# Kernel optimization log

Hardware: AMD Instinct MI355X
Metric: run time of the kernel (lower is better)

The kernel has to match this reference:

```python
import jax, jax.numpy as jnp
import numpy as np

IN_DIM, HID_DIM, OUT_DIM, HEADS = 128, 256, 128, 4
N0, N1, N2 = 80000, 40000, 8000
E1, E2 = 400000, 128000
NEG_SLOPE = 0.2


def _glorot(key, shape):
    fan = shape[0] + shape[-1]
    lim = jnp.sqrt(6.0 / fan)
    return jax.random.uniform(key, shape, jnp.float32, -lim, lim)


def setup_inputs() -> dict:
    key = jax.random.key(0)
    ks = jax.random.split(key, 16)
    inp = {
        "x": jax.random.normal(ks[0], (N0, IN_DIM), jnp.float32),
        "edge_src1": jax.random.randint(ks[1], (E1,), 0, N0),
        "edge_dst1": jax.random.randint(ks[2], (E1,), 0, N1),
        "edge_src2": jax.random.randint(ks[3], (E2,), 0, N1),
        "edge_dst2": jax.random.randint(ks[4], (E2,), 0, N2),
        # GAT1: in_dim -> heads*in_dim (shared lin for src/dst in PyG when in_channels is int)
        "W1": _glorot(ks[5], (IN_DIM, HEADS * IN_DIM)),
        "att_src1": _glorot(ks[6], (HEADS, IN_DIM)),
        "att_dst1": _glorot(ks[7], (HEADS, IN_DIM)),
        "b1": jnp.zeros((HEADS * IN_DIM,), jnp.float32),
        # GAT2: hid_dim -> hid_dim, heads=1
        "W2": _glorot(ks[8], (HID_DIM, HID_DIM)),
        "att_src2": _glorot(ks[9], (1, HID_DIM)),
        "att_dst2": _glorot(ks[10], (1, HID_DIM)),
        "b2": jnp.zeros((HID_DIM,), jnp.float32),
        # Conv1d kernel_size=1 == per-node linear
        "conv1_w": _glorot(ks[11], (HID_DIM, HEADS * IN_DIM)),
        "conv1_b": jnp.zeros((HID_DIM,), jnp.float32),
        "conv2_w": _glorot(ks[12], (OUT_DIM, HID_DIM)),
        "conv2_b": jnp.zeros((OUT_DIM,), jnp.float32),
    }
    return inp


def _gat(x_src, x_dst, src, dst, W, att_s, att_d, bias, n_dst, heads, out_c):
    h_src = (x_src @ W).reshape(-1, heads, out_c)   # [Ns,H,C]
    h_dst = (x_dst @ W).reshape(-1, heads, out_c)   # [Nd,H,C]
    a_s = jnp.einsum('nhc,hc->nh', h_src, att_s)    # [Ns,H]
    a_d = jnp.einsum('nhc,hc->nh', h_dst, att_d)    # [Nd,H]
    alpha = jax.nn.leaky_relu(a_s[src] + a_d[dst], NEG_SLOPE)  # [E,H]
    m = jax.ops.segment_max(alpha, dst, num_segments=n_dst)
    alpha = jnp.exp(alpha - jnp.maximum(m, -1e30)[dst])
    denom = jax.ops.segment_sum(alpha, dst, num_segments=n_dst)
    alpha = alpha / (denom[dst] + 1e-16)
    msg = h_src[src] * alpha[:, :, None]            # [E,H,C]
    out = jax.ops.segment_sum(msg, dst, num_segments=n_dst)
    return out.reshape(n_dst, heads * out_c) + bias


def reference(x, edge_src1, edge_dst1, edge_src2, edge_dst2,
              W1, att_src1, att_dst1, b1, W2, att_src2, att_dst2, b2,
              conv1_w, conv1_b, conv2_w, conv2_b):
    # layer 0: GAT1 (heads=4, concat) + Conv1d(512->256, k=1)
    h = _gat(x, x[:N1], edge_src1, edge_dst1, W1, att_src1, att_dst1, b1,
             N1, HEADS, IN_DIM)                      # [N1, 512]
    h = h @ conv1_w.T + conv1_b                      # [N1, 256]
    # layer 1: GAT2 (heads=1) + Conv1d(256->128, k=1)
    h = _gat(h, h[:N2], edge_src2, edge_dst2, W2, att_src2, att_dst2, b2,
             N2, 1, HID_DIM)                         # [N2, 256]
    h = h @ conv2_w.T + conv2_b                      # [N2, 128]
    return h
```

## Files before the change

kernel.cpp:

```cpp
#include <hip/hip_runtime.h>
#include <math.h>

#define IN_DIM 128
#define HID_DIM 256
#define OUT_DIM 128
#define HEADS 4
#define N0 80000
#define N1 40000
#define N2 8000
#define E1 400000
#define E2 128000
#define NEG 0.2f
#define NB1 40
#define NB2 8
#define ZERO_BLKS 47
#define PH0_BLKS (ZERO_BLKS + 4)
#define PREP_BLKS 644
#define CAST_BLKS 1250
#define HIST_BLKS 2063
#define PH1_BLKS (PREP_BLKS + CAST_BLKS + HIST_BLKS)

typedef __attribute__((ext_vector_type(8))) short bf16x8;
typedef __attribute__((ext_vector_type(4))) float f32x4;

__device__ __forceinline__ float bf2f(short s) {
  return __uint_as_float(((unsigned int)(unsigned short)s) << 16);
}
__device__ __forceinline__ short f2bf(float f) {
  unsigned int u = __float_as_uint(f);
  unsigned int r = (u + 0x7FFFu + ((u >> 16) & 1u)) >> 16;
  return (short)r;
}
__device__ __forceinline__ float lrelu(float t) {
  return t > 0.f ? t : NEG * t;
}

__global__ __launch_bounds__(256) void phase0_kernel(
    float4* __restrict__ zp, const float* __restrict__ W1,
    const float* __restrict__ att_s1, const float* __restrict__ att_d1,
    float* __restrict__ p1) {
  int b = blockIdx.x, t = threadIdx.x;
  if (b < ZERO_BLKS) {
    int i = b * 256 + t;
    if (i < 12000) zp[i] = make_float4(0.f, 0.f, 0.f, 0.f);
  } else {
    int g = (b - ZERO_BLKS) * 256 + t;
    int i = g >> 3, hh = g & 7;
    int h = hh & 3;
    const float* att = (hh < 4) ? att_s1 : att_d1;
    float acc = 0.f;
    for (int c = 0; c < 128; c++)
      acc += W1[(long)i * 512 + h * 128 + c] * att[h * 128 + c];
    p1[g] = acc;
  }
}

__global__ __launch_bounds__(256) void phase1_kernel(
    const float* __restrict__ W1, const float* __restrict__ b1,
    const float* __restrict__ c1w, const float* __restrict__ c1b,
    const float* __restrict__ W2, const float* __restrict__ att_s2,
    const float* __restrict__ att_d2, const float* __restrict__ b2,
    const float* __restrict__ c2w, const float* __restrict__ c2b,
    short* __restrict__ M1t, const float* __restrict__ p1,
    float* __restrict__ bias1p, short* __restrict__ M2t,
    float* __restrict__ p2, float* __restrict__ bias2p,
    const float* __restrict__ x, short* __restrict__ x_bf,
    float* __restrict__ a_s, float* __restrict__ a_d,
    const int* __restrict__ ed1, const int* __restrict__ ed2,
    int* __restrict__ deg1, int* __restrict__ deg2, int* __restrict__ rank1,
    int* __restrict__ rank2) {
  int b = blockIdx.x, t = threadIdx.x;
  if (b < PREP_BLKS) {
    if (b < 512) {
      int g = b * 256 + t;
      int o = g >> 9, kf = g & 511;
      int h = kf >> 7, k = kf & 127;
      float acc = 0.f;
      for (int c = 0; c < 128; c++)
        acc +=
            W1[(long)k * 512 + h * 128 + c] * c1w[(long)o * 512 + h * 128 + c];
      M1t[g] = f2bf(acc);
    } else if (b < 640) {
      int g = (b - 512) * 256 + t;
      int o = g >> 8, k = g & 255;
      float acc = 0.f;
      for (int c = 0; c < 256; c++)
        acc += W2[(long)k * 256 + c] * c2w[(long)o * 256 + c];
      M2t[g] = f2bf(acc);
    } else if (b == 640) {
      if (t < 256) {
        float acc = c1b[t];
        for (int c = 0; c < 512; c++) acc += b1[c] * c1w[(long)t * 512 + c];
        bias1p[t] = acc;
      }
    } else if (b < 643) {
      int g = (b - 641) * 256 + t;
      if (g < 512) {
        int k = g >> 1, j = g & 1;
        const float* att = j ? att_d2 : att_s2;
        float acc = 0.f;
        for (int c = 0; c < 256; c++) acc += W2[(long)k * 256 + c] * att[c];
        p2[g] = acc;
      }
    } else {
      if (t < 128) {
        float acc = c2b[t];
        for (int c = 0; c < 256; c++) acc += b2[c] * c2w[(long)t * 256 + c];
        bias2p[t] = acc;
      }
    }
  } else if (b < PREP_BLKS + CAST_BLKS) {
    int bb = b - PREP_BLKS;
    int l16 = t & 15;
    long nb = ((long)bb * 16 + (t >> 4)) * 4;
    int ch0 = l16 * 8;
    float xs[4][8];
#pragma unroll
    for (int i = 0; i < 4; i++) {
      float4 a = *(const float4*)&x[(nb + i) * 128 + ch0];
      float4 bv = *(const float4*)&x[(nb + i) * 128 + ch0 + 4];
      xs[i][0] = a.x; xs[i][1] = a.y; xs[i][2] = a.z; xs[i][3] = a.w;
      xs[i][4] = bv.x; xs[i][5] = bv.y; xs[i][6] = bv.z; xs[i][7] = bv.w;
    }
#pragma unroll
    for (int i = 0; i < 4; i++) {
      short4 o1, o2;
      o1.x = f2bf(xs[i][0]); o1.y = f2bf(xs[i][1]);
      o1.z = f2bf(xs[i][2]); o1.w = f2bf(xs[i][3]);
      o2.x = f2bf(xs[i][4]); o2.y = f2bf(xs[i][5]);
      o2.z = f2bf(xs[i][6]); o2.w = f2bf(xs[i][7]);
      *(short4*)&x_bf[(nb + i) * 128 + ch0] = o1;
      *(short4*)&x_bf[(nb + i) * 128 + ch0 + 4] = o2;
    }
    float acc[4][8] = {};
#pragma unroll
    for (int c = 0; c < 8; c++) {
      float4 pA = *(const float4*)&p1[(ch0 + c) * 8];
      float4 pB = *(const float4*)&p1[(ch0 + c) * 8 + 4];
#pragma unroll
      for (int i = 0; i < 4; i++) {
        float xc = xs[i][c];
        acc[i][0] += xc * pA.x; acc[i][1] += xc * pA.y;
        acc[i][2] += xc * pA.z; acc[i][3] += xc * pA.w;
        acc[i][4] += xc * pB.x; acc[i][5] += xc * pB.y;
        acc[i][6] += xc * pB.z; acc[i][7] += xc * pB.w;
      }
    }
#pragma unroll
    for (int off = 1; off <= 8; off <<= 1) {
#pragma unroll
      for (int i = 0; i < 4; i++)
#pragma unroll
        for (int k = 0; k < 8; k++) acc[i][k] += __shfl_xor(acc[i][k], off);
    }
    if (l16 == 0) {
#pragma unroll
      for (int i = 0; i < 4; i++) {
        long n = nb + i;
        *(float4*)&a_s[n * 4] =
            make_float4(acc[i][0], acc[i][1], acc[i][2], acc[i][3]);
        if (n < N1)
          *(float4*)&a_d[n * 4] =
              make_float4(acc[i][4], acc[i][5], acc[i][6], acc[i][7]);
      }
    }
  } else {
    int e = (b - PREP_BLKS - CAST_BLKS) * 256 + t;
    if (e < E1) {
      rank1[e] = atomicAdd(&deg1[ed1[e]], 1);
    } else {
      int e2 = e - E1;
      if (e2 < E2) rank2[e2] = atomicAdd(&deg2[ed2[e2]], 1);
    }
  }
}

template<bool BIAS, bool OUTBF>
__global__ __launch_bounds__(256) void mm_bf16_kernel(
    const short* __restrict__ A, const short* __restrict__ Bt,
    const float* __restrict__ bias, void* __restrict__ Cv,
    int M, int N, int K) {
  __shared__ short As[128][72];
  __shared__ short Bs[64][72];
  int tid = threadIdx.x;
  int bn = blockIdx.x * 64;
  int bm = blockIdx.y * 128;
  int w = tid >> 6;
  int lane = tid & 63;
  int lr = lane & 15, kb = lane >> 4;
  f32x4 acc[2][4] = {};

  for (int k0 = 0; k0 < K; k0 += 64) {
#pragma unroll
    for (int i = 0; i < 4; i++) {
      int seg = tid + i * 256;
      int row = seg >> 3, part = seg & 7;
      int gm = bm + row;
      bf16x8 v = {0, 0, 0, 0, 0, 0, 0, 0};
      if (gm < M) v = *(const bf16x8*)(A + (long)gm * K + k0 + part * 8);
      *(bf16x8*)&As[row][part * 8] = v;
    }
#pragma unroll
    for (int i = 0; i < 2; i++) {
      int seg = tid + i * 256;
      int r = seg >> 3, part = seg & 7;
      *(bf16x8*)&Bs[r][part * 8] =
          *(const bf16x8*)(Bt + (long)(bn + r) * K + k0 + part * 8);
    }
    __syncthreads();
#pragma unroll
    for (int kk = 0; kk < 64; kk += 32) {
      bf16x8 a0 = *(const bf16x8*)&As[w * 32 + lr][kk + kb * 8];
      bf16x8 a1 = *(const bf16x8*)&As[w * 32 + 16 + lr][kk + kb * 8];
      bf16x8 b0 = *(const bf16x8*)&Bs[lr][kk + kb * 8];
      bf16x8 b1 = *(const bf16x8*)&Bs[16 + lr][kk + kb * 8];
      bf16x8 b2 = *(const bf16x8*)&Bs[32 + lr][kk + kb * 8];
      bf16x8 b3 = *(const bf16x8*)&Bs[48 + lr][kk + kb * 8];
      acc[0][0] = __builtin_amdgcn_mfma_f32_16x16x32_bf16(a0, b0, acc[0][0], 0, 0, 0);
      acc[0][1] = __builtin_amdgcn_mfma_f32_16x16x32_bf16(a0, b1, acc[0][1], 0, 0, 0);
      acc[0][2] = __builtin_amdgcn_mfma_f32_16x16x32_bf16(a0, b2, acc[0][2], 0, 0, 0);
      acc[0][3] = __builtin_amdgcn_mfma_f32_16x16x32_bf16(a0, b3, acc[0][3], 0, 0, 0);
      acc[1][0] = __builtin_amdgcn_mfma_f32_16x16x32_bf16(a1, b0, acc[1][0], 0, 0, 0);
      acc[1][1] = __builtin_amdgcn_mfma_f32_16x16x32_bf16(a1, b1, acc[1][1], 0, 0, 0);
      acc[1][2] = __builtin_amdgcn_mfma_f32_16x16x32_bf16(a1, b2, acc[1][2], 0, 0, 0);
      acc[1][3] = __builtin_amdgcn_mfma_f32_16x16x32_bf16(a1, b3, acc[1][3], 0, 0, 0);
    }
    __syncthreads();
  }
#pragma unroll
  for (int mt = 0; mt < 2; mt++) {
#pragma unroll
    for (int nt = 0; nt < 4; nt++) {
#pragma unroll
      for (int r = 0; r < 4; r++) {
        int row = bm + w * 32 + mt * 16 + kb * 4 + r;
        if (row >= M) continue;
        int col = bn + nt * 16 + lr;
        float v = acc[mt][nt][r];
        if (BIAS) v += bias[col];
        if (OUTBF)
          ((short*)Cv)[(long)row * N + col] = f2bf(v);
        else
          ((float*)Cv)[(long)row * N + col] = v;
      }
    }
  }
}

__global__ __launch_bounds__(256) void attn2_kernel(
    const short* __restrict__ hid1, const float* __restrict__ p2,
    float* __restrict__ a_s, float* __restrict__ a_d) {
  int tid = threadIdx.x;
  int l32 = tid & 31;
  long n = (long)blockIdx.x * 8 + (tid >> 5);
  if (n >= N1) return;
  int ch0 = l32 * 8;
  bf16x8 hv = *(const bf16x8*)&hid1[n * 256 + ch0];
  float s = 0.f, d = 0.f;
#pragma unroll
  for (int c = 0; c < 8; c += 2) {
    float4 q = *(const float4*)&p2[(ch0 + c) * 2];
    float h0 = bf2f(hv[c]), h1 = bf2f(hv[c + 1]);
    s += h0 * q.x + h1 * q.z;
    d += h0 * q.y + h1 * q.w;
  }
#pragma unroll
  for (int off = 1; off <= 16; off <<= 1) {
    s += __shfl_xor(s, off);
    d += __shfl_xor(d, off);
  }
  if (l32 == 0) {
    a_s[n] = s;
    if (n < N2) a_d[n] = d;
  }
}

__global__ __launch_bounds__(256) void scanA12_kernel(
    const int* __restrict__ deg1, const int* __restrict__ deg2,
    int* __restrict__ part) {
  __shared__ int red[256];
  int b = blockIdx.x;
  const int* deg;
  int n, base;
  if (b < NB1) { deg = deg1; n = N1; base = b * 1024; }
  else { deg = deg2; n = N2; base = (b - NB1) * 1024; }
  int s = 0;
  for (int i = threadIdx.x; i < 1024; i += 256) {
    int idx = base + i;
    if (idx < n) s += deg[idx];
  }
  red[threadIdx.x] = s;
  __syncthreads();
  for (int off = 128; off >= 1; off >>= 1) {
    if (threadIdx.x < off) red[threadIdx.x] += red[threadIdx.x + off];
    __syncthreads();
  }
  if (threadIdx.x == 0) part[b] = red[0];
}

__global__ __launch_bounds__(256) void scanC12_kernel(
    const int* __restrict__ deg1, const int* __restrict__ deg2,
    const int* __restrict__ part, int* __restrict__ offs1,
    int* __restrict__ offs2) {
  __shared__ int tsum[256];
  int b = blockIdx.x;
  const int* deg;
  int n, pbase, bl;
  int* offs;
  if (b < NB1) { deg = deg1; n = N1; offs = offs1; pbase = 0; bl = b; }
  else { deg = deg2; n = N2; offs = offs2; pbase = NB1; bl = b - NB1; }
  int boff = 0;
  for (int i = 0; i < bl; i++) boff += part[pbase + i];
  int base = bl * 1024;
  int v[4];
  int s = 0;
#pragma unroll
  for (int k = 0; k < 4; k++) {
    int idx = base + threadIdx.x * 4 + k;
    v[k] = (idx < n) ? deg[idx] : 0;
    s += v[k];
  }
  tsum[threadIdx.x] = s;
  __syncthreads();
  for (int off = 1; off < 256; off <<= 1) {
    int t = (threadIdx.x >= off) ? tsum[threadIdx.x - off] : 0;
    __syncthreads();
    tsum[threadIdx.x] += t;
    __syncthreads();
  }
  int run = boff + ((threadIdx.x > 0) ? tsum[threadIdx.x - 1] : 0);
#pragma unroll
  for (int k = 0; k < 4; k++) {
    int idx = base + threadIdx.x * 4 + k;
    if (idx < n) {
      offs[idx] = run;
      run += v[k];
    }
  }
  if (bl == 0 && threadIdx.x == 0) offs[n] = (b < NB1) ? E1 : E2;
}

__global__ void scatter1_kernel(const int* __restrict__ src,
                                const int* __restrict__ dst, int E,
                                const int* __restrict__ offs,
                                const int* __restrict__ rank,
                                const float* __restrict__ a_s,
                                const float* __restrict__ a_d,
                                int* __restrict__ csr_src,
                                float* __restrict__ csr_w) {
  int e = blockIdx.x * blockDim.x + threadIdx.x;
  if (e >= E) return;
  int s = src[e], d = dst[e];
  int p = offs[d] + rank[e];
  csr_src[p] = s;
  float4 as = *(const float4*)&a_s[s * 4];
  float4 ad = *(const float4*)&a_d[d * 4];
  float4 t;
  t.x = __expf(lrelu(as.x + ad.x));
  t.y = __expf(lrelu(as.y + ad.y));
  t.z = __expf(lrelu(as.z + ad.z));
  t.w = __expf(lrelu(as.w + ad.w));
  *(float4*)&csr_w[(long)p * 4] = t;
}

__global__ void scatter2_kernel(const int* __restrict__ src,
                                const int* __restrict__ dst, int E,
                                const int* __restrict__ offs,
                                const int* __restrict__ rank,
                                const float* __restrict__ a_s,
                                const float* __restrict__ a_d,
                                int* __restrict__ csr_src,
                                float* __restrict__ csr_w) {
  int e = blockIdx.x * blockDim.x + threadIdx.x;
  if (e >= E) return;
  int s = src[e], d = dst[e];
  int p = offs[d] + rank[e];
  csr_src[p] = s;
  csr_w[p] = __expf(lrelu(a_s[s] + a_d[d]));
}

__global__ __launch_bounds__(256) void gather1_kernel(
    const short* __restrict__ x, const int* __restrict__ csr_src,
    const float* __restrict__ csr_w, const int* __restrict__ offs,
    short* __restrict__ z1) {
  int wid = threadIdx.x >> 6, lane = threadIdx.x & 63;
  long d = (long)blockIdx.x * 4 + wid;
  if (d >= N1) return;
  int lo = offs[d], deg = offs[d + 1] - lo;
  int half = lane >> 5, l32 = lane & 31;
  float acc[4][4] = {};
  float den[4] = {};
#pragma unroll 2
  for (int j = half; j < deg; j += 2) {
    long p = lo + j;
    int s = csr_src[p];
    float4 w = *(const float4*)&csr_w[p * 4];
    short4 xv = *(const short4*)&x[(long)s * 128 + l32 * 4];
    float f0 = bf2f(xv.x), f1 = bf2f(xv.y), f2 = bf2f(xv.z), f3 = bf2f(xv.w);
    den[0] += w.x; den[1] += w.y; den[2] += w.z; den[3] += w.w;
    acc[0][0] += w.x * f0; acc[0][1] += w.x * f1; acc[0][2] += w.x * f2; acc[0][3] += w.x * f3;
    acc[1][0] += w.y * f0; acc[1][1] += w.y * f1; acc[1][2] += w.y * f2; acc[1][3] += w.y * f3;
    acc[2][0] += w.z * f0; acc[2][1] += w.z * f1; acc[2][2] += w.z * f2; acc[2][3] += w.z * f3;
    acc[3][0] += w.w * f0; acc[3][1] += w.w * f1; acc[3][2] += w.w * f2; acc[3][3] += w.w * f3;
  }
#pragma unroll
  for (int h = 0; h < 4; h++) {
    den[h] += __shfl_xor(den[h], 32);
#pragma unroll
    for (int k = 0; k < 4; k++) acc[h][k] += __shfl_xor(acc[h][k], 32);
  }
  if (half == 0) {
#pragma unroll
    for (int h = 0; h < 4; h++) {
      float inv = 1.f / (den[h] + 1e-16f);
      short4 o;
      o.x = f2bf(acc[h][0] * inv);
      o.y = f2bf(acc[h][1] * inv);
      o.z = f2bf(acc[h][2] * inv);
      o.w = f2bf(acc[h][3] * inv);
      *(short4*)&z1[d * 512 + h * 128 + l32 * 4] = o;
    }
  }
}

__global__ __launch_bounds__(256) void gather2_kernel(
    const short* __restrict__ hid1, const int* __restrict__ csr_src,
    const float* __restrict__ csr_w, const int* __restrict__ offs,
    short* __restrict__ z2) {
  int wid = threadIdx.x >> 6, lane = threadIdx.x & 63;
  long d = (long)blockIdx.x * 4 + wid;
  if (d >= N2) return;
  int lo = offs[d], deg = offs[d + 1] - lo;
  int half = lane >> 5, l32 = lane & 31;
  int ch0 = l32 * 8;
  float acc[8] = {};
  float den = 0.f;
#pragma unroll 2
  for (int j = half; j < deg; j += 2) {
    long p = lo + j;
    int s = csr_src[p];
    float w = csr_w[p];
    den += w;
    bf16x8 v = *(const bf16x8*)&hid1[(long)s * 256 + ch0];
#pragma unroll
    for (int k = 0; k < 8; k++) acc[k] += w * bf2f(v[k]);
  }
  den += __shfl_xor(den, 32);
#pragma unroll
  for (int k = 0; k < 8; k++) acc[k] += __shfl_xor(acc[k], 32);
  if (half == 0) {
    float inv = 1.f / (den + 1e-16f);
    bf16x8 o;
#pragma unroll
    for (int k = 0; k < 8; k++) o[k] = f2bf(acc[k] * inv);
    *(bf16x8*)&z2[d * 256 + ch0] = o;
  }
}

extern "C" void kernel_launch(void* const* d_in, const int* in_sizes, int n_in,
                              void* d_out, int out_size, void* d_ws,
                              size_t ws_size, hipStream_t stream) {
  const float* x = (const float*)d_in[0];
  const int* es1 = (const int*)d_in[1];
  const int* ed1 = (const int*)d_in[2];
  const int* es2 = (const int*)d_in[3];
  const int* ed2 = (const int*)d_in[4];
  const float* W1 = (const float*)d_in[5];
  const float* att_s1 = (const float*)d_in[6];
  const float* att_d1 = (const float*)d_in[7];
  const float* b1 = (const float*)d_in[8];
  const float* W2 = (const float*)d_in[9];
  const float* att_s2 = (const float*)d_in[10];
  const float* att_d2 = (const float*)d_in[11];
  const float* b2 = (const float*)d_in[12];
  const float* c1w = (const float*)d_in[13];
  const float* c1b = (const float*)d_in[14];
  const float* c2w = (const float*)d_in[15];
  const float* c2b = (const float*)d_in[16];
  float* out = (float*)d_out;

  char* ws = (char*)d_ws;
  size_t off = 0;
  auto alloc = [&](size_t bytes) {
    void* p = ws + off;
    off += (bytes + 255) & ~(size_t)255;
    return p;
  };
  short* x_bf = (short*)alloc((size_t)N0 * 128 * 2);
  short* z1 = (short*)alloc((size_t)N1 * 512 * 2);
  short* hid1 = (short*)alloc((size_t)N1 * 256 * 2);
  short* z2 = (short*)alloc((size_t)N2 * 256 * 2);
  float* p1 = (float*)alloc(128 * 8 * 4);
  short* M1t = (short*)alloc(256 * 512 * 2);
  float* bias1p = (float*)alloc(256 * 4);
  float* p2 = (float*)alloc(256 * 2 * 4);
  short* M2t = (short*)alloc(128 * 256 * 2);
  float* bias2p = (float*)alloc(128 * 4);
  float* as1 = (float*)alloc((size_t)N0 * 4 * 4);
  float* ad1v = (float*)alloc((size_t)N1 * 4 * 4);
  float* as2 = (float*)alloc((size_t)N1 * 4);
  float* ad2v = (float*)alloc((size_t)N2 * 4);
  int* deg1 = (int*)alloc((size_t)N1 * 4);
  int* deg2 = (int*)alloc((size_t)N2 * 4);
  int* offs1 = (int*)alloc((size_t)(N1 + 1) * 4);
  int* rank1 = (int*)alloc((size_t)E1 * 4);
  int* offs2 = (int*)alloc((size_t)(N2 + 1) * 4);
  int* rank2 = (int*)alloc((size_t)E2 * 4);
  int* part12 = (int*)alloc(64 * 4);
  int* csr_src1 = (int*)alloc((size_t)E1 * 4);
  float* csr_w1 = (float*)alloc((size_t)E1 * 4 * 4);
  int* csr_src2 = (int*)alloc((size_t)E2 * 4);
  float* csr_w2 = (float*)alloc((size_t)E2 * 4);

  phase0_kernel<<<PH0_BLKS, 256, 0, stream>>>((float4*)deg1, W1, att_s1,
                                              att_d1, p1);

  phase1_kernel<<<PH1_BLKS, 256, 0, stream>>>(
      W1, b1, c1w, c1b, W2, att_s2, att_d2, b2, c2w, c2b, M1t, p1, bias1p,
      M2t, p2, bias2p, x, x_bf, as1, ad1v, ed1, ed2, deg1, deg2, rank1, rank2);

  scanA12_kernel<<<NB1 + NB2, 256, 0, stream>>>(deg1, deg2, part12);
  scanC12_kernel<<<NB1 + NB2, 256, 0, stream>>>(deg1, deg2, part12, offs1,
                                                offs2);
  scatter1_kernel<<<(E1 + 255) / 256, 256, 0, stream>>>(
      es1, ed1, E1, offs1, rank1, as1, ad1v, csr_src1, csr_w1);
  gather1_kernel<<<(N1 + 3) / 4, 256, 0, stream>>>(x_bf, csr_src1, csr_w1,
                                                   offs1, z1);
  mm_bf16_kernel<true, true><<<dim3(4, (N1 + 127) / 128), 256, 0, stream>>>(
      z1, M1t, bias1p, hid1, N1, 256, 512);

  attn2_kernel<<<(N1 + 7) / 8, 256, 0, stream>>>(hid1, p2, as2, ad2v);
  scatter2_kernel<<<(E2 + 255) / 256, 256, 0, stream>>>(
      es2, ed2, E2, offs2, rank2, as2, ad2v, csr_src2, csr_w2);
  gather2_kernel<<<(N2 + 3) / 4, 256, 0, stream>>>(hid1, csr_src2, csr_w2,
                                                   offs2, z2);
  mm_bf16_kernel<true, false><<<dim3(2, (N2 + 127) / 128), 256, 0, stream>>>(
      z2, M2t, bias2p, out, N2, 128, 256);
}
```

Baseline: 189.8 us.

## Fuse layer-2 attention logits into GEMM epilogue and widen gather1 loads

```diff
diff --git a/kernel.cpp b/kernel.cpp
--- a/kernel.cpp
+++ b/kernel.cpp
@@ -13,7 +13,7 @@
 #define NEG 0.2f
 #define NB1 40
 #define NB2 8
-#define ZERO_BLKS 47
+#define ZERO_BLKS 94
 #define PH0_BLKS (ZERO_BLKS + 4)
 #define PREP_BLKS 644
 #define CAST_BLKS 1250
@@ -42,13 +42,14 @@
   int b = blockIdx.x, t = threadIdx.x;
   if (b < ZERO_BLKS) {
     int i = b * 256 + t;
-    if (i < 12000) zp[i] = make_float4(0.f, 0.f, 0.f, 0.f);
+    if (i < 24000) zp[i] = make_float4(0.f, 0.f, 0.f, 0.f);
   } else {
     int g = (b - ZERO_BLKS) * 256 + t;
     int i = g >> 3, hh = g & 7;
     int h = hh & 3;
     const float* att = (hh < 4) ? att_s1 : att_d1;
     float acc = 0.f;
+#pragma unroll 8
     for (int c = 0; c < 128; c++)
       acc += W1[(long)i * 512 + h * 128 + c] * att[h * 128 + c];
     p1[g] = acc;
@@ -76,6 +77,7 @@
       int o = g >> 9, kf = g & 511;
       int h = kf >> 7, k = kf & 127;
       float acc = 0.f;
+#pragma unroll 8
       for (int c = 0; c < 128; c++)
         acc +=
             W1[(long)k * 512 + h * 128 + c] * c1w[(long)o * 512 + h * 128 + c];
@@ -84,12 +86,14 @@
       int g = (b - 512) * 256 + t;
       int o = g >> 8, k = g & 255;
       float acc = 0.f;
+#pragma unroll 8
       for (int c = 0; c < 256; c++)
         acc += W2[(long)k * 256 + c] * c2w[(long)o * 256 + c];
       M2t[g] = f2bf(acc);
     } else if (b == 640) {
       if (t < 256) {
         float acc = c1b[t];
+#pragma unroll 8
         for (int c = 0; c < 512; c++) acc += b1[c] * c1w[(long)t * 512 + c];
         bias1p[t] = acc;
       }
@@ -99,12 +103,14 @@
         int k = g >> 1, j = g & 1;
         const float* att = j ? att_d2 : att_s2;
         float acc = 0.f;
+#pragma unroll 8
         for (int c = 0; c < 256; c++) acc += W2[(long)k * 256 + c] * att[c];
         p2[g] = acc;
       }
     } else {
       if (t < 128) {
         float acc = c2b[t];
+#pragma unroll 8
         for (int c = 0; c < 256; c++) acc += b2[c] * c2w[(long)t * 256 + c];
         bias2p[t] = acc;
       }
@@ -175,11 +181,12 @@
   }
 }
 
-template<bool BIAS, bool OUTBF>
+template<bool BIAS, bool OUTBF, bool ATTN2>
 __global__ __launch_bounds__(256) void mm_bf16_kernel(
     const short* __restrict__ A, const short* __restrict__ Bt,
     const float* __restrict__ bias, void* __restrict__ Cv,
-    int M, int N, int K) {
+    int M, int N, int K, const float* __restrict__ p2,
+    float* __restrict__ as2, float* __restrict__ ad2v) {
   __shared__ short As[128][72];
   __shared__ short Bs[64][72];
   int tid = threadIdx.x;
@@ -227,6 +234,16 @@
     }
     __syncthreads();
   }
+  float p2s_c[4], p2d_c[4];
+  if (ATTN2) {
+#pragma unroll
+    for (int nt = 0; nt < 4; nt++) {
+      int col = bn + nt * 16 + lr;
+      p2s_c[nt] = p2[col * 2];
+      p2d_c[nt] = p2[col * 2 + 1];
+    }
+  }
+  float sp[2][4] = {}, dp[2][4] = {};
 #pragma unroll
   for (int mt = 0; mt < 2; mt++) {
 #pragma unroll
@@ -238,6 +255,10 @@
         int col = bn + nt * 16 + lr;
         float v = acc[mt][nt][r];
         if (BIAS) v += bias[col];
+        if (ATTN2) {
+          sp[mt][r] += v * p2s_c[nt];
+          dp[mt][r] += v * p2d_c[nt];
+        }
         if (OUTBF)
           ((short*)Cv)[(long)row * N + col] = f2bf(v);
         else
@@ -245,33 +266,24 @@
       }
     }
   }
-}
-
-__global__ __launch_bounds__(256) void attn2_kernel(
-    const short* __restrict__ hid1, const float* __restrict__ p2,
-    float* __restrict__ a_s, float* __restrict__ a_d) {
-  int tid = threadIdx.x;
-  int l32 = tid & 31;
-  long n = (long)blockIdx.x * 8 + (tid >> 5);
-  if (n >= N1) return;
-  int ch0 = l32 * 8;
-  bf16x8 hv = *(const bf16x8*)&hid1[n * 256 + ch0];
-  float s = 0.f, d = 0.f;
-#pragma unroll
-  for (int c = 0; c < 8; c += 2) {
-    float4 q = *(const float4*)&p2[(ch0 + c) * 2];
-    float h0 = bf2f(hv[c]), h1 = bf2f(hv[c + 1]);
-    s += h0 * q.x + h1 * q.z;
-    d += h0 * q.y + h1 * q.w;
-  }
-#pragma unroll
-  for (int off = 1; off <= 16; off <<= 1) {
-    s += __shfl_xor(s, off);
-    d += __shfl_xor(d, off);
-  }
-  if (l32 == 0) {
-    a_s[n] = s;
-    if (n < N2) a_d[n] = d;
+  if (ATTN2) {
+#pragma unroll
+    for (int mt = 0; mt < 2; mt++) {
+#pragma unroll
+      for (int r = 0; r < 4; r++) {
+        float s = sp[mt][r], dv = dp[mt][r];
+#pragma unroll
+        for (int off = 1; off <= 8; off <<= 1) {
+          s += __shfl_xor(s, off);
+          dv += __shfl_xor(dv, off);
+        }
+        int row = bm + w * 32 + mt * 16 + kb * 4 + r;
+        if (lr == 0 && row < M) {
+          atomicAdd(&as2[row], s);
+          if (row < N2) atomicAdd(&ad2v[row], dv);
+        }
+      }
+    }
   }
 }
 
@@ -387,38 +399,44 @@
   long d = (long)blockIdx.x * 4 + wid;
   if (d >= N1) return;
   int lo = offs[d], deg = offs[d + 1] - lo;
-  int half = lane >> 5, l32 = lane & 31;
-  float acc[4][4] = {};
+  int q = lane >> 4, l16 = lane & 15;
+  int ch0 = l16 * 8;
+  float acc[4][8] = {};
   float den[4] = {};
-#pragma unroll 2
-  for (int j = half; j < deg; j += 2) {
+  for (int j = q; j < deg; j += 4) {
     long p = lo + j;
     int s = csr_src[p];
     float4 w = *(const float4*)&csr_w[p * 4];
-    short4 xv = *(const short4*)&x[(long)s * 128 + l32 * 4];
-    float f0 = bf2f(xv.x), f1 = bf2f(xv.y), f2 = bf2f(xv.z), f3 = bf2f(xv.w);
+    bf16x8 xv = *(const bf16x8*)&x[(long)s * 128 + ch0];
+    float f[8];
+#pragma unroll
+    for (int k = 0; k < 8; k++) f[k] = bf2f(xv[k]);
     den[0] += w.x; den[1] += w.y; den[2] += w.z; den[3] += w.w;
-    acc[0][0] += w.x * f0; acc[0][1] += w.x * f1; acc[0][2] += w.x * f2; acc[0][3] += w.x * f3;
-    acc[1][0] += w.y * f0; acc[1][1] += w.y * f1; acc[1][2] += w.y * f2; acc[1][3] += w.y * f3;
-    acc[2][0] += w.z * f0; acc[2][1] += w.z * f1; acc[2][2] += w.z * f2; acc[2][3] += w.z * f3;
-    acc[3][0] += w.w * f0; acc[3][1] += w.w * f1; acc[3][2] += w.w * f2; acc[3][3] += w.w * f3;
-  }
-#pragma unroll
-  for (int h = 0; h < 4; h++) {
-    den[h] += __shfl_xor(den[h], 32);
-#pragma unroll
-    for (int k = 0; k < 4; k++) acc[h][k] += __shfl_xor(acc[h][k], 32);
-  }
-  if (half == 0) {
+#pragma unroll
+    for (int k = 0; k < 8; k++) {
+      acc[0][k] += w.x * f[k];
+      acc[1][k] += w.y * f[k];
+      acc[2][k] += w.z * f[k];
+      acc[3][k] += w.w * f[k];
+    }
+  }
+#pragma unroll
+  for (int off = 16; off <= 32; off <<= 1) {
+#pragma unroll
+    for (int h = 0; h < 4; h++) {
+      den[h] += __shfl_xor(den[h], off);
+#pragma unroll
+      for (int k = 0; k < 8; k++) acc[h][k] += __shfl_xor(acc[h][k], off);
+    }
+  }
+  if (q == 0) {
 #pragma unroll
     for (int h = 0; h < 4; h++) {
       float inv = 1.f / (den[h] + 1e-16f);
-      short4 o;
-      o.x = f2bf(acc[h][0] * inv);
-      o.y = f2bf(acc[h][1] * inv);
-      o.z = f2bf(acc[h][2] * inv);
-      o.w = f2bf(acc[h][3] * inv);
-      *(short4*)&z1[d * 512 + h * 128 + l32 * 4] = o;
+      bf16x8 o;
+#pragma unroll
+      for (int k = 0; k < 8; k++) o[k] = f2bf(acc[h][k] * inv);
+      *(bf16x8*)&z1[d * 512 + h * 128 + ch0] = o;
     }
   }
 }
@@ -498,10 +516,10 @@
   float* bias2p = (float*)alloc(128 * 4);
   float* as1 = (float*)alloc((size_t)N0 * 4 * 4);
   float* ad1v = (float*)alloc((size_t)N1 * 4 * 4);
+  int* deg1 = (int*)alloc((size_t)N1 * 4);
+  int* deg2 = (int*)alloc((size_t)N2 * 4);
   float* as2 = (float*)alloc((size_t)N1 * 4);
   float* ad2v = (float*)alloc((size_t)N2 * 4);
-  int* deg1 = (int*)alloc((size_t)N1 * 4);
-  int* deg2 = (int*)alloc((size_t)N2 * 4);
   int* offs1 = (int*)alloc((size_t)(N1 + 1) * 4);
   int* rank1 = (int*)alloc((size_t)E1 * 4);
   int* offs2 = (int*)alloc((size_t)(N2 + 1) * 4);
@@ -526,14 +544,16 @@
       es1, ed1, E1, offs1, rank1, as1, ad1v, csr_src1, csr_w1);
   gather1_kernel<<<(N1 + 3) / 4, 256, 0, stream>>>(x_bf, csr_src1, csr_w1,
                                                    offs1, z1);
-  mm_bf16_kernel<true, true><<<dim3(4, (N1 + 127) / 128), 256, 0, stream>>>(
-      z1, M1t, bias1p, hid1, N1, 256, 512);
-
-  attn2_kernel<<<(N1 + 7) / 8, 256, 0, stream>>>(hid1, p2, as2, ad2v);
+  mm_bf16_kernel<true, true, true><<<dim3(4, (N1 + 127) / 128), 256, 0,
+                                     stream>>>(z1, M1t, bias1p, hid1, N1, 256,
+                                               512, p2, as2, ad2v);
+
   scatter2_kernel<<<(E2 + 255) / 256, 256, 0, stream>>>(
       es2, ed2, E2, offs2, rank2, as2, ad2v, csr_src2, csr_w2);
   gather2_kernel<<<(N2 + 3) / 4, 256, 0, stream>>>(hid1, csr_src2, csr_w2,
                                                    offs2, z2);
-  mm_bf16_kernel<true, false><<<dim3(2, (N2 + 127) / 128), 256, 0, stream>>>(
-      z2, M2t, bias2p, out, N2, 128, 256);
-}
+  mm_bf16_kernel<true, false, false><<<dim3(2, (N2 + 127) / 128), 256, 0,
+                                       stream>>>(z2, M2t, bias2p, out, N2, 128,
+                                                 256, nullptr, nullptr,
+                                                 nullptr);
+}
```

Result: slower. 194.6 us (+2.5%).

## Fold layer-2 attention projection into gather1 via precomputed M1t·p2 vectors

Applied to the files above, without the earlier changes.

```diff
diff --git a/kernel.cpp b/kernel.cpp
--- a/kernel.cpp
+++ b/kernel.cpp
@@ -19,6 +19,7 @@
 #define CAST_BLKS 1250
 #define HIST_BLKS 2063
 #define PH1_BLKS (PREP_BLKS + CAST_BLKS + HIST_BLKS)
+#define SCANQ_BLKS (NB1 + NB2 + 5)
 
 typedef __attribute__((ext_vector_type(8))) short bf16x8;
 typedef __attribute__((ext_vector_type(4))) float f32x4;
@@ -247,55 +248,45 @@
   }
 }
 
-__global__ __launch_bounds__(256) void attn2_kernel(
-    const short* __restrict__ hid1, const float* __restrict__ p2,
-    float* __restrict__ a_s, float* __restrict__ a_d) {
-  int tid = threadIdx.x;
-  int l32 = tid & 31;
-  long n = (long)blockIdx.x * 8 + (tid >> 5);
-  if (n >= N1) return;
-  int ch0 = l32 * 8;
-  bf16x8 hv = *(const bf16x8*)&hid1[n * 256 + ch0];
-  float s = 0.f, d = 0.f;
-#pragma unroll
-  for (int c = 0; c < 8; c += 2) {
-    float4 q = *(const float4*)&p2[(ch0 + c) * 2];
-    float h0 = bf2f(hv[c]), h1 = bf2f(hv[c + 1]);
-    s += h0 * q.x + h1 * q.z;
-    d += h0 * q.y + h1 * q.w;
-  }
-#pragma unroll
-  for (int off = 1; off <= 16; off <<= 1) {
-    s += __shfl_xor(s, off);
-    d += __shfl_xor(d, off);
-  }
-  if (l32 == 0) {
-    a_s[n] = s;
-    if (n < N2) a_d[n] = d;
-  }
-}
-
-__global__ __launch_bounds__(256) void scanA12_kernel(
+__global__ __launch_bounds__(256) void scanAq_kernel(
     const int* __restrict__ deg1, const int* __restrict__ deg2,
-    int* __restrict__ part) {
-  __shared__ int red[256];
+    int* __restrict__ part, const short* __restrict__ M1t,
+    const float* __restrict__ p2, const float* __restrict__ bias1p,
+    float* __restrict__ q12) {
   int b = blockIdx.x;
-  const int* deg;
-  int n, base;
-  if (b < NB1) { deg = deg1; n = N1; base = b * 1024; }
-  else { deg = deg2; n = N2; base = (b - NB1) * 1024; }
-  int s = 0;
-  for (int i = threadIdx.x; i < 1024; i += 256) {
-    int idx = base + i;
-    if (idx < n) s += deg[idx];
-  }
-  red[threadIdx.x] = s;
-  __syncthreads();
-  for (int off = 128; off >= 1; off >>= 1) {
-    if (threadIdx.x < off) red[threadIdx.x] += red[threadIdx.x + off];
+  if (b < NB1 + NB2) {
+    __shared__ int red[256];
+    const int* deg;
+    int n, base;
+    if (b < NB1) { deg = deg1; n = N1; base = b * 1024; }
+    else { deg = deg2; n = N2; base = (b - NB1) * 1024; }
+    int s = 0;
+    for (int i = threadIdx.x; i < 1024; i += 256) {
+      int idx = base + i;
+      if (idx < n) s += deg[idx];
+    }
+    red[threadIdx.x] = s;
     __syncthreads();
-  }
-  if (threadIdx.x == 0) part[b] = red[0];
+    for (int off = 128; off >= 1; off >>= 1) {
+      if (threadIdx.x < off) red[threadIdx.x] += red[threadIdx.x + off];
+      __syncthreads();
+    }
+    if (threadIdx.x == 0) part[b] = red[0];
+  } else if (b < NB1 + NB2 + 4) {
+    int g = (b - NB1 - NB2) * 256 + threadIdx.x;
+    int kf = g >> 1, j = g & 1;
+    float acc = 0.f;
+    for (int o = 0; o < 256; o++)
+      acc += bf2f(M1t[(long)o * 512 + kf]) * p2[o * 2 + j];
+    q12[g] = acc;
+  } else {
+    int t = threadIdx.x;
+    if (t < 2) {
+      float acc = 0.f;
+      for (int o = 0; o < 256; o++) acc += bias1p[o] * p2[o * 2 + t];
+      q12[1024 + t] = acc;
+    }
+  }
 }
 
 __global__ __launch_bounds__(256) void scanC12_kernel(
@@ -382,7 +373,8 @@
 __global__ __launch_bounds__(256) void gather1_kernel(
     const short* __restrict__ x, const int* __restrict__ csr_src,
     const float* __restrict__ csr_w, const int* __restrict__ offs,
-    short* __restrict__ z1) {
+    short* __restrict__ z1, const float* __restrict__ q12,
+    float* __restrict__ as2, float* __restrict__ ad2v) {
   int wid = threadIdx.x >> 6, lane = threadIdx.x & 63;
   long d = (long)blockIdx.x * 4 + wid;
   if (d >= N1) return;
@@ -410,15 +402,32 @@
     for (int k = 0; k < 4; k++) acc[h][k] += __shfl_xor(acc[h][k], 32);
   }
   if (half == 0) {
+    float s2 = 0.f, d2 = 0.f;
 #pragma unroll
     for (int h = 0; h < 4; h++) {
       float inv = 1.f / (den[h] + 1e-16f);
+      float zv[4];
+#pragma unroll
+      for (int k = 0; k < 4; k++) {
+        zv[k] = acc[h][k] * inv;
+        int ch = h * 128 + l32 * 4 + k;
+        float2 qv = *(const float2*)&q12[ch * 2];
+        s2 += zv[k] * qv.x;
+        d2 += zv[k] * qv.y;
+      }
       short4 o;
-      o.x = f2bf(acc[h][0] * inv);
-      o.y = f2bf(acc[h][1] * inv);
-      o.z = f2bf(acc[h][2] * inv);
-      o.w = f2bf(acc[h][3] * inv);
+      o.x = f2bf(zv[0]); o.y = f2bf(zv[1]);
+      o.z = f2bf(zv[2]); o.w = f2bf(zv[3]);
       *(short4*)&z1[d * 512 + h * 128 + l32 * 4] = o;
+    }
+#pragma unroll
+    for (int off = 1; off <= 16; off <<= 1) {
+      s2 += __shfl_xor(s2, off);
+      d2 += __shfl_xor(d2, off);
+    }
+    if (l32 == 0) {
+      as2[d] = s2 + q12[1024];
+      if (d < N2) ad2v[d] = d2 + q12[1025];
     }
   }
 }
@@ -496,6 +505,7 @@
   float* p2 = (float*)alloc(256 * 2 * 4);
   short* M2t = (short*)alloc(128 * 256 * 2);
   float* bias2p = (float*)alloc(128 * 4);
+  float* q12 = (float*)alloc(1026 * 4);
   float* as1 = (float*)alloc((size_t)N0 * 4 * 4);
   float* ad1v = (float*)alloc((size_t)N1 * 4 * 4);
   float* as2 = (float*)alloc((size_t)N1 * 4);
@@ -519,19 +529,18 @@
       W1, b1, c1w, c1b, W2, att_s2, att_d2, b2, c2w, c2b, M1t, p1, bias1p,
       M2t, p2, bias2p, x, x_bf, as1, ad1v, ed1, ed2, deg1, deg2, rank1, rank2);
 
-  scanA12_kernel<<<NB1 + NB2, 256, 0, stream>>>(deg1, deg2, part12);
+  scanAq_kernel<<<SCANQ_BLKS, 256, 0, stream>>>(deg1, deg2, part12, M1t, p2,
+                                                bias1p, q12);
   scanC12_kernel<<<NB1 + NB2, 256, 0, stream>>>(deg1, deg2, part12, offs1,
                                                 offs2);
   scatter1_kernel<<<(E1 + 255) / 256, 256, 0, stream>>>(
       es1, ed1, E1, offs1, rank1, as1, ad1v, csr_src1, csr_w1);
   gather1_kernel<<<(N1 + 3) / 4, 256, 0, stream>>>(x_bf, csr_src1, csr_w1,
-                                                   offs1, z1);
+                                                   offs1, z1, q12, as2, ad2v);
+  scatter2_kernel<<<(E2 + 255) / 256, 256, 0, stream>>>(
+      es2, ed2, E2, offs2, rank2, as2, ad2v, csr_src2, csr_w2);
   mm_bf16_kernel<true, true><<<dim3(4, (N1 + 127) / 128), 256, 0, stream>>>(
       z1, M1t, bias1p, hid1, N1, 256, 512);
-
-  attn2_kernel<<<(N1 + 7) / 8, 256, 0, stream>>>(hid1, p2, as2, ad2v);
-  scatter2_kernel<<<(E2 + 255) / 256, 256, 0, stream>>>(
-      es2, ed2, E2, offs2, rank2, as2, ad2v, csr_src2, csr_w2);
   gather2_kernel<<<(N2 + 3) / 4, 256, 0, stream>>>(hid1, csr_src2, csr_w2,
                                                    offs2, z2);
   mm_bf16_kernel<true, false><<<dim3(2, (N2 + 127) / 128), 256, 0, stream>>>(
```

Measured after the change: 196.4 us (median of 2 runs). 1.03x slower.

## Replicate degree counters eight ways to reduce atomic contention in CSR build

Applied to the files above, without the earlier changes.

```diff
diff --git a/kernel.cpp b/kernel.cpp
--- a/kernel.cpp
+++ b/kernel.cpp
@@ -13,7 +13,8 @@
 #define NEG 0.2f
 #define NB1 40
 #define NB2 8
-#define ZERO_BLKS 47
+#define REP 8
+#define ZERO_BLKS 375
 #define PH0_BLKS (ZERO_BLKS + 4)
 #define PREP_BLKS 644
 #define CAST_BLKS 1250
@@ -42,7 +43,8 @@
   int b = blockIdx.x, t = threadIdx.x;
   if (b < ZERO_BLKS) {
     int i = b * 256 + t;
-    if (i < 12000) zp[i] = make_float4(0.f, 0.f, 0.f, 0.f);
+    if (i < (N1 + N2) * 2) zp[i] = make_float4(0.f, 0.f, 0.f, 0.f);
+    else if (i < 96000) zp[i] = make_float4(0.f, 0.f, 0.f, 0.f);
   } else {
     int g = (b - ZERO_BLKS) * 256 + t;
     int i = g >> 3, hh = g & 7;
@@ -67,8 +69,8 @@
     const float* __restrict__ x, short* __restrict__ x_bf,
     float* __restrict__ a_s, float* __restrict__ a_d,
     const int* __restrict__ ed1, const int* __restrict__ ed2,
-    int* __restrict__ deg1, int* __restrict__ deg2, int* __restrict__ rank1,
-    int* __restrict__ rank2) {
+    int* __restrict__ degR1, int* __restrict__ degR2,
+    int* __restrict__ rank1, int* __restrict__ rank2) {
   int b = blockIdx.x, t = threadIdx.x;
   if (b < PREP_BLKS) {
     if (b < 512) {
@@ -165,12 +167,13 @@
       }
     }
   } else {
+    int r = b & 7;
     int e = (b - PREP_BLKS - CAST_BLKS) * 256 + t;
     if (e < E1) {
-      rank1[e] = atomicAdd(&deg1[ed1[e]], 1);
+      rank1[e] = atomicAdd(&degR1[(long)r * N1 + ed1[e]], 1);
     } else {
       int e2 = e - E1;
-      if (e2 < E2) rank2[e2] = atomicAdd(&deg2[ed2[e2]], 1);
+      if (e2 < E2) rank2[e2] = atomicAdd(&degR2[(long)r * N2 + ed2[e2]], 1);
     }
   }
 }
@@ -276,18 +279,21 @@
 }
 
 __global__ __launch_bounds__(256) void scanA12_kernel(
-    const int* __restrict__ deg1, const int* __restrict__ deg2,
+    const int* __restrict__ degR1, const int* __restrict__ degR2,
     int* __restrict__ part) {
   __shared__ int red[256];
   int b = blockIdx.x;
   const int* deg;
   int n, base;
-  if (b < NB1) { deg = deg1; n = N1; base = b * 1024; }
-  else { deg = deg2; n = N2; base = (b - NB1) * 1024; }
+  if (b < NB1) { deg = degR1; n = N1; base = b * 1024; }
+  else { deg = degR2; n = N2; base = (b - NB1) * 1024; }
   int s = 0;
   for (int i = threadIdx.x; i < 1024; i += 256) {
     int idx = base + i;
-    if (idx < n) s += deg[idx];
+    if (idx < n) {
+#pragma unroll
+      for (int r = 0; r < REP; r++) s += deg[(long)r * n + idx];
+    }
   }
   red[threadIdx.x] = s;
   __syncthreads();
@@ -299,16 +305,18 @@
 }
 
 __global__ __launch_bounds__(256) void scanC12_kernel(
-    const int* __restrict__ deg1, const int* __restrict__ deg2,
+    const int* __restrict__ degR1, const int* __restrict__ degR2,
     const int* __restrict__ part, int* __restrict__ offs1,
-    int* __restrict__ offs2) {
+    int* __restrict__ offs2, int* __restrict__ rbase1,
+    int* __restrict__ rbase2) {
   __shared__ int tsum[256];
   int b = blockIdx.x;
   const int* deg;
   int n, pbase, bl;
   int* offs;
-  if (b < NB1) { deg = deg1; n = N1; offs = offs1; pbase = 0; bl = b; }
-  else { deg = deg2; n = N2; offs = offs2; pbase = NB1; bl = b - NB1; }
+  int* rbase;
+  if (b < NB1) { deg = degR1; n = N1; offs = offs1; rbase = rbase1; pbase = 0; bl = b; }
+  else { deg = degR2; n = N2; offs = offs2; rbase = rbase2; pbase = NB1; bl = b - NB1; }
   int boff = 0;
   for (int i = 0; i < bl; i++) boff += part[pbase + i];
   int base = bl * 1024;
@@ -317,8 +325,13 @@
 #pragma unroll
   for (int k = 0; k < 4; k++) {
     int idx = base + threadIdx.x * 4 + k;
-    v[k] = (idx < n) ? deg[idx] : 0;
-    s += v[k];
+    int tot = 0;
+    if (idx < n) {
+#pragma unroll
+      for (int r = 0; r < REP; r++) tot += deg[(long)r * n + idx];
+    }
+    v[k] = tot;
+    s += tot;
   }
   tsum[threadIdx.x] = s;
   __syncthreads();
@@ -334,6 +347,12 @@
     int idx = base + threadIdx.x * 4 + k;
     if (idx < n) {
       offs[idx] = run;
+      int acc = run;
+#pragma unroll
+      for (int r = 0; r < REP; r++) {
+        rbase[(long)idx * REP + r] = acc;
+        acc += deg[(long)r * n + idx];
+      }
       run += v[k];
     }
   }
@@ -342,7 +361,7 @@
 
 __global__ void scatter1_kernel(const int* __restrict__ src,
                                 const int* __restrict__ dst, int E,
-                                const int* __restrict__ offs,
+                                const int* __restrict__ rbase,
                                 const int* __restrict__ rank,
                                 const float* __restrict__ a_s,
                                 const float* __restrict__ a_d,
@@ -351,7 +370,8 @@
   int e = blockIdx.x * blockDim.x + threadIdx.x;
   if (e >= E) return;
   int s = src[e], d = dst[e];
-  int p = offs[d] + rank[e];
+  int r = (PREP_BLKS + CAST_BLKS + (e >> 8)) & 7;
+  int p = rbase[(long)d * REP + r] + rank[e];
   csr_src[p] = s;
   float4 as = *(const float4*)&a_s[s * 4];
   float4 ad = *(const float4*)&a_d[d * 4];
@@ -365,7 +385,7 @@
 
 __global__ void scatter2_kernel(const int* __restrict__ src,
                                 const int* __restrict__ dst, int E,
-                                const int* __restrict__ offs,
+                                const int* __restrict__ rbase,
                                 const int* __restrict__ rank,
                                 const float* __restrict__ a_s,
                                 const float* __restrict__ a_d,
@@ -374,7 +394,8 @@
   int e = blockIdx.x * blockDim.x + threadIdx.x;
   if (e >= E) return;
   int s = src[e], d = dst[e];
-  int p = offs[d] + rank[e];
+  int r = (PREP_BLKS + CAST_BLKS + ((E1 + e) >> 8)) & 7;
+  int p = rbase[(long)d * REP + r] + rank[e];
   csr_src[p] = s;
   csr_w[p] = __expf(lrelu(a_s[s] + a_d[d]));
 }
@@ -500,8 +521,10 @@
   float* ad1v = (float*)alloc((size_t)N1 * 4 * 4);
   float* as2 = (float*)alloc((size_t)N1 * 4);
   float* ad2v = (float*)alloc((size_t)N2 * 4);
-  int* deg1 = (int*)alloc((size_t)N1 * 4);
-  int* deg2 = (int*)alloc((size_t)N2 * 4);
+  int* degR1 = (int*)alloc((size_t)N1 * REP * 4);
+  int* degR2 = (int*)alloc((size_t)N2 * REP * 4);
+  int* rbase1 = (int*)alloc((size_t)N1 * REP * 4);
+  int* rbase2 = (int*)alloc((size_t)N2 * REP * 4);
   int* offs1 = (int*)alloc((size_t)(N1 + 1) * 4);
   int* rank1 = (int*)alloc((size_t)E1 * 4);
   int* offs2 = (int*)alloc((size_t)(N2 + 1) * 4);
@@ -512,18 +535,19 @@
   int* csr_src2 = (int*)alloc((size_t)E2 * 4);
   float* csr_w2 = (float*)alloc((size_t)E2 * 4);
 
-  phase0_kernel<<<PH0_BLKS, 256, 0, stream>>>((float4*)deg1, W1, att_s1,
+  phase0_kernel<<<PH0_BLKS, 256, 0, stream>>>((float4*)degR1, W1, att_s1,
                                               att_d1, p1);
 
   phase1_kernel<<<PH1_BLKS, 256, 0, stream>>>(
       W1, b1, c1w, c1b, W2, att_s2, att_d2, b2, c2w, c2b, M1t, p1, bias1p,
-      M2t, p2, bias2p, x, x_bf, as1, ad1v, ed1, ed2, deg1, deg2, rank1, rank2);
-
-  scanA12_kernel<<<NB1 + NB2, 256, 0, stream>>>(deg1, deg2, part12);
-  scanC12_kernel<<<NB1 + NB2, 256, 0, stream>>>(deg1, deg2, part12, offs1,
-                                                offs2);
+      M2t, p2, bias2p, x, x_bf, as1, ad1v, ed1, ed2, degR1, degR2, rank1,
+      rank2);
+
+  scanA12_kernel<<<NB1 + NB2, 256, 0, stream>>>(degR1, degR2, part12);
+  scanC12_kernel<<<NB1 + NB2, 256, 0, stream>>>(degR1, degR2, part12, offs1,
+                                                offs2, rbase1, rbase2);
   scatter1_kernel<<<(E1 + 255) / 256, 256, 0, stream>>>(
-      es1, ed1, E1, offs1, rank1, as1, ad1v, csr_src1, csr_w1);
+      es1, ed1, E1, rbase1, rank1, as1, ad1v, csr_src1, csr_w1);
   gather1_kernel<<<(N1 + 3) / 4, 256, 0, stream>>>(x_bf, csr_src1, csr_w1,
                                                    offs1, z1);
   mm_bf16_kernel<true, true><<<dim3(4, (N1 + 127) / 128), 256, 0, stream>>>(
@@ -531,7 +555,7 @@
 
   attn2_kernel<<<(N1 + 7) / 8, 256, 0, stream>>>(hid1, p2, as2, ad2v);
   scatter2_kernel<<<(E2 + 255) / 256, 256, 0, stream>>>(
-      es2, ed2, E2, offs2, rank2, as2, ad2v, csr_src2, csr_w2);
+      es2, ed2, E2, rbase2, rank2, as2, ad2v, csr_src2, csr_w2);
   gather2_kernel<<<(N2 + 3) / 4, 256, 0, stream>>>(hid1, csr_src2, csr_w2,
                                                    offs2, z2);
   mm_bf16_kernel<true, false><<<dim3(2, (N2 + 127) / 128), 256, 0, stream>>>(
```

After: 190.0 us. No clear change (+0.1%).
